# Optimization experiments

Measured on AMD Instinct MI355X. Metric: run time of the kernel, lower is better.

The kernel has to match this reference:

```python
import jax, jax.numpy as jnp
import numpy as np

N = 100_000      # nodes
E = 800_000      # edges (avg degree 8)
IN = 64          # in_channels
OUT = 64         # out_channels
HEADS = 4
HD = OUT // HEADS  # per-head out channels (concat=True)


def _unif(key, shape, fan_in):
    b = 1.0 / np.sqrt(fan_in)
    return jax.random.uniform(key, shape, jnp.float32, -b, b)


def setup_inputs() -> dict:
    key = jax.random.key(0)
    ks = jax.random.split(key, 12)
    x = jax.random.normal(ks[0], (N, IN), jnp.float32)
    pos = jax.random.normal(ks[1], (N, 3), jnp.float32)
    edge_index = jax.random.randint(ks[2], (2, E), 0, N, jnp.int32)
    # Per-head PointTransformerConv params (stacked over heads).
    # lin / lin_src / lin_dst are bias-free Linear(in, hd); pos_nn is Linear(3, hd) with bias.
    W_lin = _unif(ks[3], (HEADS, IN, HD), IN)
    W_src = _unif(ks[4], (HEADS, IN, HD), IN)
    W_dst = _unif(ks[5], (HEADS, IN, HD), IN)
    W_pos = _unif(ks[6], (HEADS, 3, HD), 3)
    b_pos = _unif(ks[7], (HEADS, HD), 3)
    # projection MLP: Linear(OUT,OUT) -> ReLU -> Linear(OUT,OUT)
    W1 = _unif(ks[8], (OUT, OUT), OUT)
    b1 = _unif(ks[9], (OUT,), OUT)
    W2 = _unif(ks[10], (OUT, OUT), OUT)
    b2 = _unif(ks[11], (OUT,), OUT)
    return dict(x=x, pos=pos, edge_index=edge_index, W_lin=W_lin, W_src=W_src,
                W_dst=W_dst, W_pos=W_pos, b_pos=b_pos, W1=W1, b1=b1, W2=W2, b2=b2)


def reference(x, pos, edge_index, W_lin, W_src, W_dst, W_pos, b_pos, W1, b1, W2, b2):
    # Add self-loops (PointTransformerConv default add_self_loops=True).
    loops = jnp.arange(N, dtype=edge_index.dtype)
    src = jnp.concatenate([edge_index[0], loops])   # j (source)
    dst = jnp.concatenate([edge_index[1], loops])   # i (target)

    # Per-node, all-heads projections: [N, H, HD]
    v = jnp.einsum('ni,hio->nho', x, W_lin)
    a_src = jnp.einsum('ni,hio->nho', x, W_src)
    a_dst = jnp.einsum('ni,hio->nho', x, W_dst)

    # Relative-position encoding delta = pos_nn(pos_i - pos_j): [Et, H, HD]
    rel = pos[dst] - pos[src]
    delta = jnp.einsum('ec,hco->eho', rel, W_pos) + b_pos

    # Attention logits per edge/channel: alpha_i - alpha_j + delta
    alpha = a_dst[dst] - a_src[src] + delta

    # Segment softmax over incoming edges of each target node (numerically stable).
    amax = jax.ops.segment_max(alpha, dst, num_segments=N)
    amax = jnp.where(jnp.isfinite(amax), amax, 0.0)
    ex = jnp.exp(alpha - amax[dst])
    denom = jax.ops.segment_sum(ex, dst, num_segments=N)
    attn = ex / jnp.maximum(denom[dst], 1e-16)

    # Message = attn * (lin(x_j) + delta), scatter-sum to targets: [N, H, HD]
    msg = attn * (v[src] + delta)
    out_h = jax.ops.segment_sum(msg, dst, num_segments=N)

    # Concat heads -> projection MLP
    out = out_h.reshape(N, HEADS * HD)
    h = jax.nn.relu(out @ W1 + b1)
    return h @ W2 + b2
```

## Files before the change

kernel.cpp:

```cpp
#include <hip/hip_runtime.h>
#include <math.h>


typedef _Float16 f16;
typedef _Float16 f16x2 __attribute__((ext_vector_type(2)));
typedef _Float16 f16x4 __attribute__((ext_vector_type(4)));
typedef _Float16 f16x8 __attribute__((ext_vector_type(8)));
typedef float f32x4 __attribute__((ext_vector_type(4)));

#define A_PITCH 104
#define C_PITCH 200
#define LOG2E 1.44269504f
#define S_CAP 32

__global__ __launch_bounds__(256) void prep_hist_scatter_kernel(
    const int* __restrict__ ei, int E, int Hb,
    int* __restrict__ cnt, int* __restrict__ ssrc,
    const float* __restrict__ Ws, const float* __restrict__ Wl,
    const float* __restrict__ Wp, const float* __restrict__ bp,
    const float* __restrict__ W1, const float* __restrict__ W2,
    f16* __restrict__ Bt, f16* __restrict__ W1p, f16* __restrict__ W2p)
{
    if ((int)blockIdx.x < Hb) {
        int e = blockIdx.x * 256 + threadIdx.x;
        if (e < E) {
            int s = ei[e], d = ei[E + e];
            int r = atomicAdd(&cnt[d], 1);
            if (r < S_CAP) ssrc[d * S_CAP + r] = s;
        }
        return;
    }
    int idx = (blockIdx.x - Hb) * 256 + threadIdx.x;
    if (idx < 192 * 96) {
        int col = idx / 96, k = idx - col * 96;
        float v = 0.f;
        if (col < 128) {
            int p = col >> 1, h = p >> 4, o = p & 15;
            if (col & 1) {
                if (k < 64)      v = Wl[h * 1024 + k * 16 + o];
                else if (k < 67) v = -Wp[h * 48 + (k - 64) * 16 + o];
            } else {
                if (k < 64)      v = -LOG2E * Ws[h * 1024 + k * 16 + o];
                else if (k < 67) v = -LOG2E * Wp[h * 48 + (k - 64) * 16 + o];
            }
        } else {
            int c = col - 128, h = c >> 4, o = c & 15;
            if (k >= 64 && k < 67) v = Wp[h * 48 + (k - 64) * 16 + o];
            else if (k == 67)      v = bp[c];
        }
        Bt[col * 96 + k] = (f16)v;
    } else if (idx < 192 * 96 + 4096) {
        int t = idx - 192 * 96;
        int col = t >> 6, k = t & 63;
        W1p[col * 64 + k] = (f16)W1[k * 64 + col];
    } else if (idx < 192 * 96 + 8192) {
        int t = idx - 192 * 96 - 4096;
        int col = t >> 6, k = t & 63;
        W2p[col * 64 + k] = (f16)W2[k * 64 + col];
    }
}

__global__ __launch_bounds__(256) void gemm_kernel(
    const float* __restrict__ x, const float* __restrict__ pos,
    const f16* __restrict__ Bt,
    f16* __restrict__ AV, f16* __restrict__ G, int N)
{
    __shared__ f16 smem[64 * C_PITCH];
    int tid = threadIdx.x;
    int l = tid & 63, wv = tid >> 6;
    int quad = l >> 4, lr = l & 15;
    int nb = blockIdx.x * 64;

    for (int it = 0; it < 4; it++) {
        int q = it * 256 + tid;
        int n = q >> 4, k = (q & 15) * 4;
        float4 xv = make_float4(0.f, 0.f, 0.f, 0.f);
        if (nb + n < N) xv = *(const float4*)&x[(size_t)(nb + n) * 64 + k];
        f16x4 h4; h4[0] = (f16)xv.x; h4[1] = (f16)xv.y; h4[2] = (f16)xv.z; h4[3] = (f16)xv.w;
        *(f16x4*)&smem[n * A_PITCH + k] = h4;
    }
    {
        int n = tid >> 2, seg = tid & 3;
        f16x4 z = {(f16)0, (f16)0, (f16)0, (f16)0};
        f16x4 h4 = z;
        if (seg == 0 && nb + n < N) {
            h4[0] = (f16)pos[(size_t)(nb + n) * 3 + 0];
            h4[1] = (f16)pos[(size_t)(nb + n) * 3 + 1];
            h4[2] = (f16)pos[(size_t)(nb + n) * 3 + 2];
            h4[3] = (f16)1.0f;
        }
        *(f16x4*)&smem[n * A_PITCH + 64 + seg * 8] = h4;
        *(f16x4*)&smem[n * A_PITCH + 64 + seg * 8 + 4] = z;
    }
    __syncthreads();

    f16x8 af[4][3];
    #pragma unroll
    for (int mt = 0; mt < 4; mt++)
        #pragma unroll
        for (int kt = 0; kt < 3; kt++)
            af[mt][kt] = *(const f16x8*)&smem[(mt * 16 + lr) * A_PITCH + kt * 32 + quad * 8];
    __syncthreads();

    #pragma unroll
    for (int t = 0; t < 3; t++) {
        int colBase = (wv * 3 + t) * 16;
        f16x8 b0 = *(const f16x8*)&Bt[(colBase + lr) * 96 + 0  + quad * 8];
        f16x8 b1 = *(const f16x8*)&Bt[(colBase + lr) * 96 + 32 + quad * 8];
        f16x8 b2 = *(const f16x8*)&Bt[(colBase + lr) * 96 + 64 + quad * 8];
        #pragma unroll
        for (int mt = 0; mt < 4; mt++) {
            f32x4 acc = {0.f, 0.f, 0.f, 0.f};
            acc = __builtin_amdgcn_mfma_f32_16x16x32_f16(af[mt][0], b0, acc, 0, 0, 0);
            acc = __builtin_amdgcn_mfma_f32_16x16x32_f16(af[mt][1], b1, acc, 0, 0, 0);
            acc = __builtin_amdgcn_mfma_f32_16x16x32_f16(af[mt][2], b2, acc, 0, 0, 0);
            int col = colBase + lr;
            #pragma unroll
            for (int r = 0; r < 4; r++) {
                int row = mt * 16 + quad * 4 + r;
                smem[row * C_PITCH + col] = (f16)acc[r];
            }
        }
    }
    __syncthreads();

    for (int it = 0; it < 4; it++) {
        int cid = it * 256 + tid;
        int row = cid >> 4, off = (cid & 15) * 8;
        if (nb + row < N)
            *(f16x8*)&AV[(size_t)(nb + row) * 128 + off] =
                *(const f16x8*)&smem[row * C_PITCH + off];
    }
    for (int it = 0; it < 2; it++) {
        int cid = it * 256 + tid;
        int row = cid >> 3, off = (cid & 7) * 8;
        if (nb + row < N)
            *(f16x8*)&G[(size_t)(nb + row) * 64 + off] =
                *(const f16x8*)&smem[row * C_PITCH + 128 + off];
    }
}

__global__ __launch_bounds__(256) void attn_mlp_kernel(
    const f16* __restrict__ AV, const f16* __restrict__ G,
    const int* __restrict__ cnt, const int* __restrict__ ssrc,
    const f16* __restrict__ W1p, const f16* __restrict__ W2p,
    const float* __restrict__ b1, const float* __restrict__ b2,
    float* __restrict__ out, int N)
{
    __shared__ f16 As[32 * 72];
    __shared__ f16 Hs[32 * 72];
    int tid = threadIdx.x, c = tid & 63, wv = tid >> 6;
    int quad = c >> 4, lr = c & 15;
    int nb = blockIdx.x * 32;

    const f16x2* AV2 = (const f16x2*)AV;

    for (int t = 0; t < 8; t++) {
        int i = __builtin_amdgcn_readfirstlane(nb + wv * 8 + t);
        float oh = 0.f;
        if (i < N) {
            float Gi = (float)G[(size_t)i * 64 + c];
            f16x2 wi = AV2[(size_t)i * 64 + c];
            float e0 = __builtin_amdgcn_exp2f((float)wi[0]);
            float num = e0 * (float)wi[1];
            float den = e0;
            int deg = __builtin_amdgcn_readfirstlane(cnt[i]);
            if (deg > S_CAP) deg = S_CAP;
            int base = i * S_CAP;
            for (int k = 0; k < deg; k += 4) {
                int j0 = __builtin_amdgcn_readfirstlane(ssrc[base + k]);
                int j1 = __builtin_amdgcn_readfirstlane(ssrc[base + k + 1]);
                int j2 = __builtin_amdgcn_readfirstlane(ssrc[base + k + 2]);
                int j3 = __builtin_amdgcn_readfirstlane(ssrc[base + k + 3]);
                f16x2 w0 = AV2[(size_t)j0 * 64 + c];
                f16x2 w1 = AV2[(size_t)j1 * 64 + c];
                f16x2 w2 = AV2[(size_t)j2 * 64 + c];
                f16x2 w3 = AV2[(size_t)j3 * 64 + c];
                float e;
                e = __builtin_amdgcn_exp2f((float)w0[0]);
                num = fmaf(e, (float)w0[1], num); den += e;
                e = __builtin_amdgcn_exp2f((float)w1[0]);
                e = (k + 1 < deg) ? e : 0.f;
                num = fmaf(e, (float)w1[1], num); den += e;
                e = __builtin_amdgcn_exp2f((float)w2[0]);
                e = (k + 2 < deg) ? e : 0.f;
                num = fmaf(e, (float)w2[1], num); den += e;
                e = __builtin_amdgcn_exp2f((float)w3[0]);
                e = (k + 3 < deg) ? e : 0.f;
                num = fmaf(e, (float)w3[1], num); den += e;
            }
            oh = num / den + Gi;
        }
        As[(wv * 8 + t) * 72 + c] = (f16)oh;
    }
    __syncthreads();

    f16x8 af[2][2];
    #pragma unroll
    for (int mt = 0; mt < 2; mt++)
        #pragma unroll
        for (int kt = 0; kt < 2; kt++)
            af[mt][kt] = *(const f16x8*)&As[(mt * 16 + lr) * 72 + kt * 32 + quad * 8];

    int col = wv * 16 + lr;
    f16x8 wb0 = *(const f16x8*)&W1p[col * 64 + quad * 8];
    f16x8 wb1 = *(const f16x8*)&W1p[col * 64 + 32 + quad * 8];
    float bias1 = b1[col];
    #pragma unroll
    for (int mt = 0; mt < 2; mt++) {
        f32x4 acc = {0.f, 0.f, 0.f, 0.f};
        acc = __builtin_amdgcn_mfma_f32_16x16x32_f16(af[mt][0], wb0, acc, 0, 0, 0);
        acc = __builtin_amdgcn_mfma_f32_16x16x32_f16(af[mt][1], wb1, acc, 0, 0, 0);
        #pragma unroll
        for (int r = 0; r < 4; r++) {
            int row = mt * 16 + quad * 4 + r;
            Hs[row * 72 + col] = (f16)fmaxf(acc[r] + bias1, 0.f);
        }
    }
    __syncthreads();

    f16x8 ag[2][2];
    #pragma unroll
    for (int mt = 0; mt < 2; mt++)
        #pragma unroll
        for (int kt = 0; kt < 2; kt++)
            ag[mt][kt] = *(const f16x8*)&Hs[(mt * 16 + lr) * 72 + kt * 32 + quad * 8];

    f16x8 wc0 = *(const f16x8*)&W2p[col * 64 + quad * 8];
    f16x8 wc1 = *(const f16x8*)&W2p[col * 64 + 32 + quad * 8];
    float bias2 = b2[col];
    #pragma unroll
    for (int mt = 0; mt < 2; mt++) {
        f32x4 acc = {0.f, 0.f, 0.f, 0.f};
        acc = __builtin_amdgcn_mfma_f32_16x16x32_f16(ag[mt][0], wc0, acc, 0, 0, 0);
        acc = __builtin_amdgcn_mfma_f32_16x16x32_f16(ag[mt][1], wc1, acc, 0, 0, 0);
        #pragma unroll
        for (int r = 0; r < 4; r++) {
            int row = nb + mt * 16 + quad * 4 + r;
            if (row < N) out[(size_t)row * 64 + col] = acc[r] + bias2;
        }
    }
}

extern "C" void kernel_launch(void* const* d_in, const int* in_sizes, int n_in,
                              void* d_out, int out_size, void* d_ws, size_t ws_size,
                              hipStream_t stream)
{
    const float* x    = (const float*)d_in[0];
    const float* pos  = (const float*)d_in[1];
    const int*   ei   = (const int*)d_in[2];
    const float* Wl   = (const float*)d_in[3];
    const float* Ws   = (const float*)d_in[4];
    const float* Wp   = (const float*)d_in[6];
    const float* bpos = (const float*)d_in[7];
    const float* W1   = (const float*)d_in[8];
    const float* b1   = (const float*)d_in[9];
    const float* W2   = (const float*)d_in[10];
    const float* b2   = (const float*)d_in[11];
    float* out = (float*)d_out;

    const int N = in_sizes[0] / 64;
    const int E = in_sizes[2] / 2;

    char* w = (char*)d_ws;
    f16*  AV   = (f16*)w;                   w += (size_t)N * 128 * 2;
    f16*  G    = (f16*)w;                   w += (size_t)N * 64 * 2;
    f16*  Bt   = (f16*)w;                   w += 192 * 96 * 2;
    f16*  W1p  = (f16*)w;                   w += 4096 * 2;
    f16*  W2p  = (f16*)w;                   w += 4096 * 2;
    int*  cnt  = (int*)w;                   w += (size_t)N * 4;
    int*  ssrc = (int*)w;                   w += (size_t)N * S_CAP * 4;

    const int Hb = (E + 255) / 256;
    const int Pb = (192 * 96 + 8192 + 255) / 256;

    hipMemsetAsync(cnt, 0, (size_t)N * (1 + S_CAP) * sizeof(int), stream);

    prep_hist_scatter_kernel<<<Hb + Pb, 256, 0, stream>>>(
        ei, E, Hb, cnt, ssrc, Ws, Wl, Wp, bpos, W1, W2, Bt, W1p, W2p);
    gemm_kernel<<<(N + 63) / 64, 256, 0, stream>>>(x, pos, Bt, AV, G, N);
    attn_mlp_kernel<<<(N + 31) / 32, 256, 0, stream>>>(AV, G, cnt, ssrc, W1p, W2p,
                                                       b1, b2, out, N);
}
```

Before: 205.4 us.

## Fuse edge histogram into GEMM launch, zero only counts, batch-load neighbor indices

The hipMemset is replaced by a small kernel that clears only the count array, not the whole ssrc buffer. That kernel also does the weight prep. The edge histogram/scatter blocks move into the GEMM launch so the atomics run alongside the projection GEMM. The attention loop now loads all 32 neighbour slots with one vector load per wavefront and broadcasts each with readlane, unrolled by 8. This cuts the scalar index loads. Uninitialised ssrc slots are clamped into range and masked out by deg.

New measurement: 219.6 us. 1.07x slower.

```diff
diff --git a/kernel.cpp b/kernel.cpp
--- a/kernel.cpp
+++ b/kernel.cpp
@@ -13,24 +13,23 @@
 #define LOG2E 1.44269504f
 #define S_CAP 32
 
-__global__ __launch_bounds__(256) void prep_hist_scatter_kernel(
-    const int* __restrict__ ei, int E, int Hb,
-    int* __restrict__ cnt, int* __restrict__ ssrc,
+__global__ __launch_bounds__(256) void zero_wprep_kernel(
+    int Zb, int* __restrict__ cnt, int N,
     const float* __restrict__ Ws, const float* __restrict__ Wl,
     const float* __restrict__ Wp, const float* __restrict__ bp,
     const float* __restrict__ W1, const float* __restrict__ W2,
     f16* __restrict__ Bt, f16* __restrict__ W1p, f16* __restrict__ W2p)
 {
-    if ((int)blockIdx.x < Hb) {
-        int e = blockIdx.x * 256 + threadIdx.x;
-        if (e < E) {
-            int s = ei[e], d = ei[E + e];
-            int r = atomicAdd(&cnt[d], 1);
-            if (r < S_CAP) ssrc[d * S_CAP + r] = s;
+    if ((int)blockIdx.x < Zb) {
+        int i4 = (blockIdx.x * 256 + threadIdx.x) * 4;
+        if (i4 + 3 < N) {
+            *(int4*)&cnt[i4] = make_int4(0, 0, 0, 0);
+        } else {
+            for (int i = i4; i < N; i++) cnt[i] = 0;
         }
         return;
     }
-    int idx = (blockIdx.x - Hb) * 256 + threadIdx.x;
+    int idx = (blockIdx.x - Zb) * 256 + threadIdx.x;
     if (idx < 192 * 96) {
         int col = idx / 96, k = idx - col * 96;
         float v = 0.f;
@@ -60,13 +59,26 @@
     }
 }
 
-__global__ __launch_bounds__(256) void gemm_kernel(
+__global__ __launch_bounds__(256) void gemm_hist_kernel(
     const float* __restrict__ x, const float* __restrict__ pos,
     const f16* __restrict__ Bt,
-    f16* __restrict__ AV, f16* __restrict__ G, int N)
+    f16* __restrict__ AV, f16* __restrict__ G, int N, int Gb,
+    const int* __restrict__ ei, int E,
+    int* __restrict__ cnt, int* __restrict__ ssrc)
 {
     __shared__ f16 smem[64 * C_PITCH];
     int tid = threadIdx.x;
+
+    if ((int)blockIdx.x >= Gb) {
+        int e = (blockIdx.x - Gb) * 256 + tid;
+        if (e < E) {
+            int s = ei[e], d = ei[E + e];
+            int r = atomicAdd(&cnt[d], 1);
+            if (r < S_CAP) ssrc[d * S_CAP + r] = s;
+        }
+        return;
+    }
+
     int l = tid & 63, wv = tid >> 6;
     int quad = l >> 4, lr = l & 15;
     int nb = blockIdx.x * 64;
@@ -167,27 +179,21 @@
             int deg = __builtin_amdgcn_readfirstlane(cnt[i]);
             if (deg > S_CAP) deg = S_CAP;
             int base = i * S_CAP;
-            for (int k = 0; k < deg; k += 4) {
-                int j0 = __builtin_amdgcn_readfirstlane(ssrc[base + k]);
-                int j1 = __builtin_amdgcn_readfirstlane(ssrc[base + k + 1]);
-                int j2 = __builtin_amdgcn_readfirstlane(ssrc[base + k + 2]);
-                int j3 = __builtin_amdgcn_readfirstlane(ssrc[base + k + 3]);
-                f16x2 w0 = AV2[(size_t)j0 * 64 + c];
-                f16x2 w1 = AV2[(size_t)j1 * 64 + c];
-                f16x2 w2 = AV2[(size_t)j2 * 64 + c];
-                f16x2 w3 = AV2[(size_t)j3 * 64 + c];
-                float e;
-                e = __builtin_amdgcn_exp2f((float)w0[0]);
-                num = fmaf(e, (float)w0[1], num); den += e;
-                e = __builtin_amdgcn_exp2f((float)w1[0]);
-                e = (k + 1 < deg) ? e : 0.f;
-                num = fmaf(e, (float)w1[1], num); den += e;
-                e = __builtin_amdgcn_exp2f((float)w2[0]);
-                e = (k + 2 < deg) ? e : 0.f;
-                num = fmaf(e, (float)w2[1], num); den += e;
-                e = __builtin_amdgcn_exp2f((float)w3[0]);
-                e = (k + 3 < deg) ? e : 0.f;
-                num = fmaf(e, (float)w3[1], num); den += e;
+            int jv = ssrc[base + (c & 31)];
+            jv = jv < 0 ? 0 : (jv >= N ? N - 1 : jv);
+            #pragma unroll
+            for (int k0 = 0; k0 < S_CAP; k0 += 8) {
+                if (k0 < deg) {
+                    #pragma unroll
+                    for (int s = 0; s < 8; s++) {
+                        int j = __builtin_amdgcn_readlane(jv, k0 + s);
+                        f16x2 w = AV2[(size_t)j * 64 + c];
+                        float e = __builtin_amdgcn_exp2f((float)w[0]);
+                        e = (k0 + s < deg) ? e : 0.f;
+                        num = fmaf(e, (float)w[1], num);
+                        den += e;
+                    }
+                }
             }
             oh = num / den + Gi;
         }
@@ -271,14 +277,15 @@
     int*  cnt  = (int*)w;                   w += (size_t)N * 4;
     int*  ssrc = (int*)w;                   w += (size_t)N * S_CAP * 4;
 
+    const int Zb = (N + 1023) / 1024;
+    const int Pb = (192 * 96 + 8192 + 255) / 256;
+    const int Gb = (N + 63) / 64;
     const int Hb = (E + 255) / 256;
-    const int Pb = (192 * 96 + 8192 + 255) / 256;
-
-    hipMemsetAsync(cnt, 0, (size_t)N * (1 + S_CAP) * sizeof(int), stream);
-
-    prep_hist_scatter_kernel<<<Hb + Pb, 256, 0, stream>>>(
-        ei, E, Hb, cnt, ssrc, Ws, Wl, Wp, bpos, W1, W2, Bt, W1p, W2p);
-    gemm_kernel<<<(N + 63) / 64, 256, 0, stream>>>(x, pos, Bt, AV, G, N);
+
+    zero_wprep_kernel<<<Zb + Pb, 256, 0, stream>>>(Zb, cnt, N, Ws, Wl, Wp, bpos,
+                                                   W1, W2, Bt, W1p, W2p);
+    gemm_hist_kernel<<<Gb + Hb, 256, 0, stream>>>(x, pos, Bt, AV, G, N, Gb,
+                                                  ei, E, cnt, ssrc);
     attn_mlp_kernel<<<(N + 31) / 32, 256, 0, stream>>>(AV, G, cnt, ssrc, W1p, W2p,
                                                        b1, b2, out, N);
 }
```
